# Kernel optimization log

Hardware: AMD Instinct MI355X
Metric: run time of the kernel (lower is better)

## Reference

```python
import jax, jax.numpy as jnp
import numpy as np

B, T, KQ, KT, NDOF = 1024, 1024, 15, 20, 7


def huber(x, delta=1.0):
    ax = jnp.abs(x)
    return jnp.where(ax < delta, 0.5 * x * x, delta * (ax - 0.5 * delta))


def setup_inputs() -> dict:
    key = jax.random.key(0)
    ks = jax.random.split(key, 12)
    q_cps = jax.random.normal(ks[0], (B, KQ, NDOF), dtype=jnp.float32)
    # time-spline control points must be positive so dtau_dt > 0
    t_cps = jax.random.uniform(ks[1], (B, KT, 1), dtype=jnp.float32) + 0.5
    # B-spline basis matrices for q(tau): [1, T, KQ]
    N = jax.random.normal(ks[2], (1, T, KQ), dtype=jnp.float32)
    dN = jax.random.normal(ks[3], (1, T, KQ), dtype=jnp.float32)
    ddN = jax.random.normal(ks[4], (1, T, KQ), dtype=jnp.float32)
    dddN = jax.random.normal(ks[5], (1, T, KQ), dtype=jnp.float32)
    # time-spline basis: Nt nonnegative so dtau_dt stays positive
    Nt = jax.random.uniform(ks[6], (1, T, KT), dtype=jnp.float32)
    dNt = jax.random.normal(ks[7], (1, T, KT), dtype=jnp.float32)
    ddNt = jax.random.normal(ks[8], (1, T, KT), dtype=jnp.float32)
    q_dot_limits = jnp.array([1.4835, 1.4835, 1.7453, 1.3090, 2.2689, 2.3562, 2.3562], dtype=jnp.float32)
    q_ddot_limits = 10.0 * q_dot_limits
    q_dddot_limits = 100.0 * q_dot_limits
    torque_limits = jnp.array([320.0, 320.0, 176.0, 176.0, 110.0, 40.0, 40.0], dtype=jnp.float32)
    return {"q_cps": q_cps, "t_cps": t_cps, "N": N, "dN": dN, "ddN": ddN,
            "dddN": dddN, "Nt": Nt, "dNt": dNt, "ddNt": ddNt,
            "q_dot_limits": q_dot_limits, "q_ddot_limits": q_ddot_limits,
            "q_dddot_limits": q_dddot_limits, "torque_limits": torque_limits}


def reference(q_cps, t_cps, N, dN, ddN, dddN, Nt, dNt, ddNt,
              q_dot_limits, q_ddot_limits, q_dddot_limits, torque_limits):
    # spline evaluations: [B, T, NDOF] and [B, T, 1]
    q = jnp.einsum('ijk,lkm->ljm', N, q_cps)
    q_dot_tau = jnp.einsum('ijk,lkm->ljm', dN, q_cps)
    q_ddot_tau = jnp.einsum('ijk,lkm->ljm', ddN, q_cps)
    q_dddot_tau = jnp.einsum('ijk,lkm->ljm', dddN, q_cps)
    dtau_dt = jnp.einsum('ijk,lkm->ljm', Nt, t_cps)
    ddtau_dtt = jnp.einsum('ijk,lkm->ljm', dNt, t_cps)
    dddtau_dttt = jnp.einsum('ijk,lkm->ljm', ddNt, t_cps)

    dt = 1.0 / dtau_dt[..., 0] / dtau_dt.shape[1]  # [B, T]
    t_cumsum = jnp.cumsum(dt, axis=-1)
    t = jnp.sum(dt, axis=-1)

    dtau_dt2 = dtau_dt ** 2
    q_dot = q_dot_tau * dtau_dt
    q_ddot = q_ddot_tau * dtau_dt2 + ddtau_dtt * q_dot_tau * dtau_dt
    q_dddot = (q_dddot_tau * dtau_dt ** 3
               + 3.0 * q_ddot_tau * ddtau_dtt * dtau_dt2
               + q_dot_tau * dtau_dt2 * dddtau_dttt
               + q_dot_tau * ddtau_dtt ** 2 * dtau_dt)

    # original rnea() returns zeros as the forward torque value
    torque = jnp.zeros_like(q)

    dt_e = dt[..., None]  # [B, T, 1]
    torque_loss = jnp.sum(huber(jax.nn.relu(jnp.abs(torque) - torque_limits)) * dt_e, axis=1)
    q_dot_loss = jnp.sum(huber(jax.nn.relu(jnp.abs(q_dot) - q_dot_limits)) * dt_e, axis=1)
    q_ddot_loss = jnp.sum(huber(jax.nn.relu(jnp.abs(q_ddot) - q_ddot_limits)) * dt_e, axis=1)
    q_dddot_loss = jnp.sum(huber(jax.nn.relu(jnp.abs(q_dddot) - q_dddot_limits)) * dt_e, axis=1)

    model_losses = jnp.concatenate([q_dot_loss, q_ddot_loss, q_dddot_loss], axis=-1)
    model_loss = jnp.sum(model_losses)
    return (model_loss, q_dot_loss, q_ddot_loss, q_dddot_loss, torque_loss,
            q, q_dot, q_ddot, q_dddot, torque, t, t_cumsum, dt)
```

## Files before the change

kernel.cpp:

```cpp
#include <hip/hip_runtime.h>

#define BB 1024
#define TT 1024
#define KQ 15
#define KT 20
#define KTP 21
#define NDOF 7
#define TTILE 64
#define NTTILE (TT/TTILE)
#define BW 4
#define NBGRP (BB/BW)

#define OFF_MODEL 0
#define OFF_QDL   1
#define OFF_QDDL  (1 + BB*NDOF)
#define OFF_QDDDL (1 + 2*BB*NDOF)
#define OFF_TQL   (1 + 3*BB*NDOF)
#define OFF_Q     (1 + 4*BB*NDOF)
#define OFF_QD    (OFF_Q    + (size_t)BB*TT*NDOF)
#define OFF_QDD   (OFF_QD   + (size_t)BB*TT*NDOF)
#define OFF_QDDD  (OFF_QDD  + (size_t)BB*TT*NDOF)
#define OFF_TQ    (OFF_QDDD + (size_t)BB*TT*NDOF)
#define OFF_T     (OFF_TQ   + (size_t)BB*TT*NDOF)
#define OFF_TCUM  (OFF_T    + (size_t)BB)
#define OFF_DT    (OFF_TCUM + (size_t)BB*TT)

__device__ __forceinline__ float hub(float v, float lim) {
    float x = fabsf(v) - lim;
    x = fmaxf(x, 0.0f);
    return (x < 1.0f) ? 0.5f * x * x : (x - 0.5f);
}

__device__ __forceinline__ void st4(float* p, float x0, float x1, float x2, float x3) {
    float v[4] = {x0, x1, x2, x3};
    __builtin_memcpy(p, v, 16);
}

__global__ __launch_bounds__(256, 4) void feas_main(
    const float* __restrict__ q_cps, const float* __restrict__ t_cps,
    const float* __restrict__ Nb,  const float* __restrict__ dNb,
    const float* __restrict__ ddNb, const float* __restrict__ dddNb,
    const float* __restrict__ Ntb, const float* __restrict__ dNtb,
    const float* __restrict__ ddNtb,
    const float* __restrict__ qd_lim, const float* __restrict__ qdd_lim,
    const float* __restrict__ qddd_lim,
    float* __restrict__ out)
{
    const int ttile = blockIdx.x;
    const int bgrp  = blockIdx.y;
    const int tid   = threadIdx.x;
    const int lane  = tid & 63;
    const int w     = tid >> 6;
    const int bw = __builtin_amdgcn_readfirstlane(bgrp * BW + w);

    __shared__ __align__(16) float qb[4 * TTILE * KQ];
    __shared__ float tb[3 * TTILE * KTP];
    __shared__ float lred[BW * 21];

    {
        const size_t gq = (size_t)ttile * TTILE * KQ;
        if (tid < 240) {
            const float4 v0 = *(const float4*)(Nb    + gq + tid * 4);
            const float4 v1 = *(const float4*)(dNb   + gq + tid * 4);
            const float4 v2 = *(const float4*)(ddNb  + gq + tid * 4);
            const float4 v3 = *(const float4*)(dddNb + gq + tid * 4);
            *(float4*)(qb + 0 * TTILE * KQ + tid * 4) = v0;
            *(float4*)(qb + 1 * TTILE * KQ + tid * 4) = v1;
            *(float4*)(qb + 2 * TTILE * KQ + tid * 4) = v2;
            *(float4*)(qb + 3 * TTILE * KQ + tid * 4) = v3;
        }
        const size_t gt = (size_t)ttile * TTILE * KT;
        #pragma unroll
        for (int j = 0; j < 5; ++j) {
            const unsigned g = (unsigned)(j * 256 + tid);
            const unsigned t = g / 20u;
            const unsigned k = g - t * 20u;
            const unsigned l = t * KTP + k;
            tb[0 * TTILE * KTP + l] = Ntb [gt + g];
            tb[1 * TTILE * KTP + l] = dNtb[gt + g];
            tb[2 * TTILE * KTP + l] = ddNtb[gt + g];
        }
    }
    __syncthreads();

    const float* cps = q_cps + (size_t)bw * KQ * NDOF;
    const float* tcp = t_cps + (size_t)bw * KT;

    float dtau = 0.f, ddtau = 0.f, dddtau = 0.f;
    {
        const float* p = tb + lane * KTP;
        #pragma unroll
        for (int k = 0; k < KT; ++k) {
            const float tc = tcp[k];
            dtau   = fmaf(p[k],                  tc, dtau);
            ddtau  = fmaf(p[1 * TTILE * KTP + k], tc, ddtau);
            dddtau = fmaf(p[2 * TTILE * KTP + k], tc, dddtau);
        }
    }

    float aq[NDOF], a1[NDOF], a2[NDOF], a3[NDOF];
    #pragma unroll
    for (int d = 0; d < NDOF; ++d) { aq[d] = 0.f; a1[d] = 0.f; a2[d] = 0.f; a3[d] = 0.f; }
    {
        const float* p = qb + lane * KQ;
        #pragma unroll
        for (int k = 0; k < KQ; ++k) {
            const float n0 = p[k];
            const float n1 = p[1 * TTILE * KQ + k];
            const float n2 = p[2 * TTILE * KQ + k];
            const float n3 = p[3 * TTILE * KQ + k];
            #pragma unroll
            for (int d = 0; d < NDOF; ++d) {
                const float cc = cps[k * NDOF + d];
                aq[d] = fmaf(n0, cc, aq[d]);
                a1[d] = fmaf(n1, cc, a1[d]);
                a2[d] = fmaf(n2, cc, a2[d]);
                a3[d] = fmaf(n3, cc, a3[d]);
            }
        }
    }

    const float dtau2 = dtau * dtau;
    const float dtau3 = dtau2 * dtau;
    const float dtv   = 1.0f / (dtau * (float)TT);

    float qd[NDOF], qdd[NDOF], qddd[NDOF];
    #pragma unroll
    for (int d = 0; d < NDOF; ++d) {
        qd[d]   = a1[d] * dtau;
        qdd[d]  = a2[d] * dtau2 + ddtau * a1[d] * dtau;
        qddd[d] = a3[d] * dtau3 + 3.0f * a2[d] * ddtau * dtau2
                + a1[d] * dtau2 * dddtau + a1[d] * ddtau * ddtau * dtau;
    }

    {
        const size_t ob = (size_t)bw * (TT * NDOF) + (size_t)(ttile * TTILE + lane) * NDOF;
        st4(out + OFF_Q    + ob,     aq[0],   aq[1],   aq[2],   aq[3]);
        st4(out + OFF_Q    + ob + 3, aq[3],   aq[4],   aq[5],   aq[6]);
        st4(out + OFF_QD   + ob,     qd[0],   qd[1],   qd[2],   qd[3]);
        st4(out + OFF_QD   + ob + 3, qd[3],   qd[4],   qd[5],   qd[6]);
        st4(out + OFF_QDD  + ob,     qdd[0],  qdd[1],  qdd[2],  qdd[3]);
        st4(out + OFF_QDD  + ob + 3, qdd[3],  qdd[4],  qdd[5],  qdd[6]);
        st4(out + OFF_QDDD + ob,     qddd[0], qddd[1], qddd[2], qddd[3]);
        st4(out + OFF_QDDD + ob + 3, qddd[3], qddd[4], qddd[5], qddd[6]);
        st4(out + OFF_TQ   + ob,     0.f, 0.f, 0.f, 0.f);
        st4(out + OFF_TQ   + ob + 3, 0.f, 0.f, 0.f, 0.f);
        out[OFF_DT + (size_t)bw * TT + ttile * TTILE + lane] = dtv;
    }

    float ls[21];
    #pragma unroll
    for (int d = 0; d < NDOF; ++d) {
        ls[d]          = hub(qd[d],   qd_lim[d])   * dtv;
        ls[NDOF + d]   = hub(qdd[d],  qdd_lim[d])  * dtv;
        ls[2*NDOF + d] = hub(qddd[d], qddd_lim[d]) * dtv;
    }
    #pragma unroll
    for (int j = 0; j < 21; ++j) {
        float v = ls[j];
        #pragma unroll
        for (int off = 32; off > 0; off >>= 1) v += __shfl_down(v, off);
        ls[j] = v;
    }
    if (lane == 0) {
        #pragma unroll
        for (int j = 0; j < 21; ++j) lred[w * 21 + j] = ls[j];
    }
    __syncthreads();
    if (tid < BW * 21) {
        const int wv = tid / 21, j = tid - wv * 21;
        const int which = j / NDOF, d = j - which * NDOF;
        const size_t o = (which == 0) ? (size_t)OFF_QDL
                       : (which == 1) ? (size_t)OFF_QDDL : (size_t)OFF_QDDDL;
        atomicAdd(out + o + (size_t)(bgrp * BW + wv) * NDOF + d, lred[tid]);
    }
    if (tid == 0) {
        float s = 0.f;
        #pragma unroll
        for (int j = 0; j < BW * 21; ++j) s += lred[j];
        atomicAdd(out + OFF_MODEL, s);
    }
}

__global__ __launch_bounds__(256) void feas_scan(float* __restrict__ out)
{
    __shared__ float sb[TT];
    __shared__ float seg[256];
    const int b   = blockIdx.x;
    const int tid = threadIdx.x;

    const int s4 = 4 * tid;
    const size_t dtb = OFF_DT + (size_t)b * TT;
    const float d0 = out[dtb + s4 + 0];
    const float d1 = out[dtb + s4 + 1];
    const float d2 = out[dtb + s4 + 2];
    const float d3 = out[dtb + s4 + 3];
    const float c0 = d0;
    const float c1 = c0 + d1;
    const float c2 = c1 + d2;
    const float c3 = c2 + d3;

    seg[tid] = c3;
    __syncthreads();
    #pragma unroll
    for (int off = 1; off < 256; off <<= 1) {
        float v = 0.0f;
        if (tid >= off) v = seg[tid - off];
        __syncthreads();
        if (tid >= off) seg[tid] += v;
        __syncthreads();
    }
    const float excl  = (tid > 0) ? seg[tid - 1] : 0.0f;
    const float total = seg[255];

    sb[s4 + 0] = c0 + excl;
    sb[s4 + 1] = c1 + excl;
    sb[s4 + 2] = c2 + excl;
    sb[s4 + 3] = c3 + excl;
    __syncthreads();
    const size_t tb = OFF_TCUM + (size_t)b * TT;
    #pragma unroll
    for (int j = 0; j < 4; ++j) {
        const int f = j * 256 + tid;
        out[tb + f] = sb[f];
    }
    if (tid == 0) out[OFF_T + b] = total;
}

extern "C" void kernel_launch(void* const* d_in, const int* in_sizes, int n_in,
                              void* d_out, int out_size, void* d_ws, size_t ws_size,
                              hipStream_t stream) {
    const float* q_cps    = (const float*)d_in[0];
    const float* t_cps    = (const float*)d_in[1];
    const float* Nb       = (const float*)d_in[2];
    const float* dNb      = (const float*)d_in[3];
    const float* ddNb     = (const float*)d_in[4];
    const float* dddNb    = (const float*)d_in[5];
    const float* Ntb      = (const float*)d_in[6];
    const float* dNtb     = (const float*)d_in[7];
    const float* ddNtb    = (const float*)d_in[8];
    const float* qd_lim   = (const float*)d_in[9];
    const float* qdd_lim  = (const float*)d_in[10];
    const float* qddd_lim = (const float*)d_in[11];
    float* out = (float*)d_out;

    hipMemsetAsync(d_out, 0, (size_t)OFF_Q * sizeof(float), stream);
    feas_main<<<dim3(NTTILE, NBGRP), dim3(256), 0, stream>>>(
        q_cps, t_cps, Nb, dNb, ddNb, dddNb, Ntb, dNtb, ddNtb,
        qd_lim, qdd_lim, qddd_lim, out);
    feas_scan<<<dim3(BB), dim3(256), 0, stream>>>(out);
}
```

Baseline: 230.3 us.

## Stage outputs through LDS for coalesced stores and drop atomics for deterministic reductions

Before the global write, each wave's per-timestep q, q_dot, q_ddot and q_dddot values are staged in shared memory. They are then written as contiguous float4 rows, which replaces the overlapping strided stores. The loss partial sums, which atomics used to accumulate, are written per tile to a workspace. The scan kernel now reduces them, and a tiny final kernel sums the model loss, so the memset is no longer needed. The change adds a third kernel launch, more workspace traffic and a lower occupancy hint.

```diff
diff --git a/kernel.cpp b/kernel.cpp
--- a/kernel.cpp
+++ b/kernel.cpp
@@ -25,6 +25,9 @@
 #define OFF_TCUM  (OFF_T    + (size_t)BB)
 #define OFF_DT    (OFF_TCUM + (size_t)BB*TT)
 
+#define WS_LOSS   0
+#define WS_BSUM   ((size_t)BB * NTTILE * 21)
+
 __device__ __forceinline__ float hub(float v, float lim) {
     float x = fabsf(v) - lim;
     x = fmaxf(x, 0.0f);
@@ -36,7 +39,7 @@
     __builtin_memcpy(p, v, 16);
 }
 
-__global__ __launch_bounds__(256, 4) void feas_main(
+__global__ __launch_bounds__(256, 2) void feas_main(
     const float* __restrict__ q_cps, const float* __restrict__ t_cps,
     const float* __restrict__ Nb,  const float* __restrict__ dNb,
     const float* __restrict__ ddNb, const float* __restrict__ dddNb,
@@ -44,7 +47,7 @@
     const float* __restrict__ ddNtb,
     const float* __restrict__ qd_lim, const float* __restrict__ qdd_lim,
     const float* __restrict__ qddd_lim,
-    float* __restrict__ out)
+    float* __restrict__ out, float* __restrict__ lws)
 {
     const int ttile = blockIdx.x;
     const int bgrp  = blockIdx.y;
@@ -53,12 +56,12 @@
     const int w     = tid >> 6;
     const int bw = __builtin_amdgcn_readfirstlane(bgrp * BW + w);
 
-    __shared__ __align__(16) float qb[4 * TTILE * KQ];
-    __shared__ float tb[3 * TTILE * KTP];
-    __shared__ float lred[BW * 21];
-
-    {
-        const size_t gq = (size_t)ttile * TTILE * KQ;
+    __shared__ __align__(16) float smem[3840 + 3 * TTILE * KTP];
+    float* qb = smem;
+    float* tb = smem + 3840;
+
+    {
+        const size_t gq = (size_t)ttile * (TTILE * KQ);
         if (tid < 240) {
             const float4 v0 = *(const float4*)(Nb    + gq + tid * 4);
             const float4 v1 = *(const float4*)(dNb   + gq + tid * 4);
@@ -69,7 +72,7 @@
             *(float4*)(qb + 2 * TTILE * KQ + tid * 4) = v2;
             *(float4*)(qb + 3 * TTILE * KQ + tid * 4) = v3;
         }
-        const size_t gt = (size_t)ttile * TTILE * KT;
+        const size_t gt = (size_t)ttile * (TTILE * KT);
         #pragma unroll
         for (int j = 0; j < 5; ++j) {
             const unsigned g = (unsigned)(j * 256 + tid);
@@ -92,7 +95,7 @@
         #pragma unroll
         for (int k = 0; k < KT; ++k) {
             const float tc = tcp[k];
-            dtau   = fmaf(p[k],                  tc, dtau);
+            dtau   = fmaf(p[k],                   tc, dtau);
             ddtau  = fmaf(p[1 * TTILE * KTP + k], tc, ddtau);
             dddtau = fmaf(p[2 * TTILE * KTP + k], tc, dddtau);
         }
@@ -133,59 +136,68 @@
                 + a1[d] * dtau2 * dddtau + a1[d] * ddtau * ddtau * dtau;
     }
 
-    {
-        const size_t ob = (size_t)bw * (TT * NDOF) + (size_t)(ttile * TTILE + lane) * NDOF;
-        st4(out + OFF_Q    + ob,     aq[0],   aq[1],   aq[2],   aq[3]);
-        st4(out + OFF_Q    + ob + 3, aq[3],   aq[4],   aq[5],   aq[6]);
-        st4(out + OFF_QD   + ob,     qd[0],   qd[1],   qd[2],   qd[3]);
-        st4(out + OFF_QD   + ob + 3, qd[3],   qd[4],   qd[5],   qd[6]);
-        st4(out + OFF_QDD  + ob,     qdd[0],  qdd[1],  qdd[2],  qdd[3]);
-        st4(out + OFF_QDD  + ob + 3, qdd[3],  qdd[4],  qdd[5],  qdd[6]);
-        st4(out + OFF_QDDD + ob,     qddd[0], qddd[1], qddd[2], qddd[3]);
-        st4(out + OFF_QDDD + ob + 3, qddd[3], qddd[4], qddd[5], qddd[6]);
-        st4(out + OFF_TQ   + ob,     0.f, 0.f, 0.f, 0.f);
-        st4(out + OFF_TQ   + ob + 3, 0.f, 0.f, 0.f, 0.f);
-        out[OFF_DT + (size_t)bw * TT + ttile * TTILE + lane] = dtv;
-    }
-
-    float ls[21];
-    #pragma unroll
-    for (int d = 0; d < NDOF; ++d) {
-        ls[d]          = hub(qd[d],   qd_lim[d])   * dtv;
-        ls[NDOF + d]   = hub(qdd[d],  qdd_lim[d])  * dtv;
-        ls[2*NDOF + d] = hub(qddd[d], qddd_lim[d]) * dtv;
-    }
-    #pragma unroll
-    for (int j = 0; j < 21; ++j) {
-        float v = ls[j];
-        #pragma unroll
-        for (int off = 32; off > 0; off >>= 1) v += __shfl_down(v, off);
-        ls[j] = v;
-    }
-    if (lane == 0) {
-        #pragma unroll
-        for (int j = 0; j < 21; ++j) lred[w * 21 + j] = ls[j];
-    }
-    __syncthreads();
-    if (tid < BW * 21) {
-        const int wv = tid / 21, j = tid - wv * 21;
-        const int which = j / NDOF, d = j - which * NDOF;
-        const size_t o = (which == 0) ? (size_t)OFF_QDL
-                       : (which == 1) ? (size_t)OFF_QDDL : (size_t)OFF_QDDDL;
-        atomicAdd(out + o + (size_t)(bgrp * BW + wv) * NDOF + d, lred[tid]);
-    }
-    if (tid == 0) {
-        float s = 0.f;
-        #pragma unroll
-        for (int j = 0; j < BW * 21; ++j) s += lred[j];
-        atomicAdd(out + OFF_MODEL, s);
-    }
-}
-
-__global__ __launch_bounds__(256) void feas_scan(float* __restrict__ out)
+    out[OFF_DT + (size_t)bw * TT + ttile * TTILE + lane] = dtv;
+
+    {
+        float ls[21];
+        #pragma unroll
+        for (int d = 0; d < NDOF; ++d) {
+            ls[d]          = hub(qd[d],   qd_lim[d])   * dtv;
+            ls[NDOF + d]   = hub(qdd[d],  qdd_lim[d])  * dtv;
+            ls[2*NDOF + d] = hub(qddd[d], qddd_lim[d]) * dtv;
+        }
+        #pragma unroll
+        for (int j = 0; j < 21; ++j) {
+            float v = ls[j];
+            #pragma unroll
+            for (int off = 32; off > 0; off >>= 1) v += __shfl_down(v, off);
+            ls[j] = v;
+        }
+        if (lane == 0) {
+            float* wp = lws + WS_LOSS + ((size_t)bw * NTTILE + ttile) * 21;
+            #pragma unroll
+            for (int j = 0; j < 21; ++j) wp[j] = ls[j];
+        }
+    }
+
+    __syncthreads();
+    {
+        float* r = smem + (size_t)(w * 4) * (TTILE * NDOF) + lane * NDOF;
+        #pragma unroll
+        for (int d = 0; d < NDOF; ++d) {
+            r[0 * TTILE * NDOF + d] = aq[d];
+            r[1 * TTILE * NDOF + d] = qd[d];
+            r[2 * TTILE * NDOF + d] = qdd[d];
+            r[3 * TTILE * NDOF + d] = qddd[d];
+        }
+    }
+    __syncthreads();
+    {
+        const size_t gb = (size_t)bw * (TT * NDOF) + (size_t)ttile * (TTILE * NDOF);
+        const float* rb = smem + (size_t)(w * 4) * (TTILE * NDOF);
+        #pragma unroll
+        for (int a = 0; a < 4; ++a) {
+            const size_t off = (a == 0) ? (size_t)OFF_Q : (a == 1) ? (size_t)OFF_QD
+                             : (a == 2) ? (size_t)OFF_QDD : (size_t)OFF_QDDD;
+            const float* s = rb + a * (TTILE * NDOF);
+            const float4 x0 = *(const float4*)(s + lane * 4);
+            st4(out + off + gb + lane * 4, x0.x, x0.y, x0.z, x0.w);
+            if (lane < 48) {
+                const float4 x1 = *(const float4*)(s + 256 + lane * 4);
+                st4(out + off + gb + 256 + lane * 4, x1.x, x1.y, x1.z, x1.w);
+            }
+        }
+        st4(out + OFF_TQ + gb + lane * 4, 0.f, 0.f, 0.f, 0.f);
+        if (lane < 48) st4(out + OFF_TQ + gb + 256 + lane * 4, 0.f, 0.f, 0.f, 0.f);
+    }
+}
+
+__global__ __launch_bounds__(256) void feas_scan(
+    float* __restrict__ out, const float* __restrict__ lws, float* __restrict__ bsum)
 {
     __shared__ float sb[TT];
     __shared__ float seg[256];
+    __shared__ float lsum[21];
     const int b   = blockIdx.x;
     const int tid = threadIdx.x;
 
@@ -217,14 +229,51 @@
     sb[s4 + 1] = c1 + excl;
     sb[s4 + 2] = c2 + excl;
     sb[s4 + 3] = c3 + excl;
-    __syncthreads();
+
+    if (tid < 21) {
+        const float* wp = lws + WS_LOSS + (size_t)b * NTTILE * 21 + tid;
+        float s = 0.f;
+        #pragma unroll
+        for (int tt = 0; tt < NTTILE; ++tt) s += wp[tt * 21];
+        const int which = tid / NDOF, d = tid - which * NDOF;
+        const size_t o = (which == 0) ? (size_t)OFF_QDL
+                       : (which == 1) ? (size_t)OFF_QDDL : (size_t)OFF_QDDDL;
+        out[o + (size_t)b * NDOF + d] = s;
+        lsum[tid] = s;
+    }
+    if (tid < NDOF) out[OFF_TQL + (size_t)b * NDOF + tid] = 0.0f;
+    __syncthreads();
+
     const size_t tb = OFF_TCUM + (size_t)b * TT;
     #pragma unroll
     for (int j = 0; j < 4; ++j) {
         const int f = j * 256 + tid;
         out[tb + f] = sb[f];
     }
-    if (tid == 0) out[OFF_T + b] = total;
+    if (tid == 0) {
+        out[OFF_T + b] = total;
+        float p = 0.f;
+        #pragma unroll
+        for (int j = 0; j < 21; ++j) p += lsum[j];
+        bsum[b] = p;
+    }
+}
+
+__global__ __launch_bounds__(256) void feas_final(
+    const float* __restrict__ bsum, float* __restrict__ out)
+{
+    __shared__ float wsums[4];
+    const int tid  = threadIdx.x;
+    const int lane = tid & 63;
+    const int w    = tid >> 6;
+    float v = 0.f;
+    #pragma unroll
+    for (int j = 0; j < 4; ++j) v += bsum[j * 256 + tid];
+    #pragma unroll
+    for (int off = 32; off > 0; off >>= 1) v += __shfl_down(v, off);
+    if (lane == 0) wsums[w] = v;
+    __syncthreads();
+    if (tid == 0) out[OFF_MODEL] = wsums[0] + wsums[1] + wsums[2] + wsums[3];
 }
 
 extern "C" void kernel_launch(void* const* d_in, const int* in_sizes, int n_in,
@@ -243,10 +292,11 @@
     const float* qdd_lim  = (const float*)d_in[10];
     const float* qddd_lim = (const float*)d_in[11];
     float* out = (float*)d_out;
-
-    hipMemsetAsync(d_out, 0, (size_t)OFF_Q * sizeof(float), stream);
+    float* lws = (float*)d_ws;
+
     feas_main<<<dim3(NTTILE, NBGRP), dim3(256), 0, stream>>>(
         q_cps, t_cps, Nb, dNb, ddNb, dddNb, Ntb, dNtb, ddNtb,
-        qd_lim, qdd_lim, qddd_lim, out);
-    feas_scan<<<dim3(BB), dim3(256), 0, stream>>>(out);
-}
+        qd_lim, qdd_lim, qddd_lim, out, lws);
+    feas_scan<<<dim3(BB), dim3(256), 0, stream>>>(out, lws, lws + WS_BSUM);
+    feas_final<<<dim3(1), dim3(256), 0, stream>>>(lws + WS_BSUM, out);
+}
```

Result: faster. 225.7 us (-2.0%).
